# Kernel tuning notes

Hardware: AMD Instinct MI355X
Metric: run time of the kernel (lower is better)

The kernel has to match this reference:

```python
import jax, jax.numpy as jnp
import numpy as np

D_MODEL = 1024
N_HEADS = 16
HEAD_DIM = D_MODEL // N_HEADS
HIDDEN = 4096
EPS = 1e-5


def setup_inputs() -> dict:
    key = jax.random.key(0)
    ks = jax.random.split(key, 16)
    s = 1.0 / np.sqrt(D_MODEL)
    sh = 1.0 / np.sqrt(HIDDEN)
    inp = {
        'x': jax.random.normal(ks[0], (4, 2048, D_MODEL), dtype=jnp.float32),
        'Wq': jax.random.normal(ks[1], (D_MODEL, D_MODEL), dtype=jnp.float32) * s,
        'bq': jnp.zeros((D_MODEL,), jnp.float32),
        'Wk': jax.random.normal(ks[2], (D_MODEL, D_MODEL), dtype=jnp.float32) * s,
        'bk': jnp.zeros((D_MODEL,), jnp.float32),
        'Wv': jax.random.normal(ks[3], (D_MODEL, D_MODEL), dtype=jnp.float32) * s,
        'bv': jnp.zeros((D_MODEL,), jnp.float32),
        'Wo': jax.random.normal(ks[4], (D_MODEL, D_MODEL), dtype=jnp.float32) * s,
        'bo': jnp.zeros((D_MODEL,), jnp.float32),
        'gamma1': jnp.ones((D_MODEL,), jnp.float32),
        'beta1': jnp.zeros((D_MODEL,), jnp.float32),
        'W1': jax.random.normal(ks[5], (D_MODEL, HIDDEN), dtype=jnp.float32) * s,
        'b1': jnp.zeros((HIDDEN,), jnp.float32),
        'W2': jax.random.normal(ks[6], (HIDDEN, D_MODEL), dtype=jnp.float32) * sh,
        'b2': jnp.zeros((D_MODEL,), jnp.float32),
        'gamma2': jnp.ones((D_MODEL,), jnp.float32),
        'beta2': jnp.zeros((D_MODEL,), jnp.float32),
    }
    return inp


def _layernorm(x, gamma, beta):
    mu = jnp.mean(x, axis=-1, keepdims=True)
    var = jnp.mean(jnp.square(x - mu), axis=-1, keepdims=True)
    return (x - mu) * jax.lax.rsqrt(var + EPS) * gamma + beta


def _encoder_layer(x, Wq, bq, Wk, bk, Wv, bv, Wo, bo, gamma1, beta1,
                   W1, b1, W2, b2, gamma2, beta2):
    B, S, _ = x.shape
    # projections -> [B, H, S, Dh]
    def split_heads(t):
        return t.reshape(B, S, N_HEADS, HEAD_DIM).transpose(0, 2, 1, 3)
    q = split_heads(x @ Wq + bq)
    k = split_heads(x @ Wk + bk)
    v = split_heads(x @ Wv + bv)
    scale = 1.0 / jnp.sqrt(jnp.float32(HEAD_DIM))
    scores = jnp.einsum('bhqd,bhkd->bhqk', q, k) * scale
    attn = jax.nn.softmax(scores, axis=-1)
    ctx = jnp.einsum('bhqk,bhkd->bhqd', attn, v)
    ctx = ctx.transpose(0, 2, 1, 3).reshape(B, S, D_MODEL)
    attn_out = ctx @ Wo + bo
    # post-norm residual 1
    h = _layernorm(x + attn_out, gamma1, beta1)
    # MLP with exact (erf) GELU, as torch F.gelu default
    mlp = jax.nn.gelu(h @ W1 + b1, approximate=False) @ W2 + b2
    return _layernorm(h + mlp, gamma2, beta2)


def reference(x, Wq, bq, Wk, bk, Wv, bv, Wo, bo, gamma1, beta1,
              W1, b1, W2, b2, gamma2, beta2):
    return _encoder_layer(x, Wq, bq, Wk, bk, Wv, bv, Wo, bo, gamma1, beta1,
                          W1, b1, W2, b2, gamma2, beta2)
```

## Files before the change

### kernel.cpp

```cpp
#include <hip/hip_runtime.h>
#include <cstdint>
#include <cstddef>

using u16 = unsigned short;
using bf16x8 = __attribute__((ext_vector_type(8))) short;
using f32x4  = __attribute__((ext_vector_type(4))) float;

__device__ __forceinline__ u16 f2bf(float f) {
    union { float f; unsigned u; } v; v.f = f;
    unsigned r = v.u + 0x7fffu + ((v.u >> 16) & 1u);
    return (u16)(r >> 16);
}

__device__ __forceinline__ unsigned cvtpk(float lo, float hi) {
    unsigned r;
    asm("v_cvt_pk_bf16_f32 %0, %1, %2" : "=v"(r) : "v"(lo), "v"(hi));
    return r;
}

__device__ __forceinline__ float fexp2(float x) {
    float r;
    asm("v_exp_f32 %0, %1" : "=v"(r) : "v"(x));
    return r;
}

__device__ __forceinline__ float gelu_f(float x) {
    const float t2 = fminf(x * fmaf(0.10294825f, x * x, 2.3022082f), 80.f);
    const float e  = fexp2(t2);
    return x * e * __frcp_rn(e + 1.0f);
}

__device__ __forceinline__ void gld_lds16(const void* g, void* l) {
    __builtin_amdgcn_global_load_lds(
        (__attribute__((address_space(1))) void*)g,
        (__attribute__((address_space(3))) void*)l, 16, 0, 0);
}

__device__ __forceinline__ f32x4 mfma16(bf16x8 a, bf16x8 b, f32x4 c) {
    return __builtin_amdgcn_mfma_f32_16x16x32_bf16(a, b, c, 0, 0, 0);
}

__global__ __launch_bounds__(256)
void cast_kernel(const float* __restrict__ in, u16* __restrict__ out, int n8) {
    int i = blockIdx.x * 256 + threadIdx.x;
    if (i >= n8) return;
    const float4* p = (const float4*)in;
    float4 a = p[i * 2], b = p[i * 2 + 1];
    ushort4 r0 = make_ushort4(f2bf(a.x), f2bf(a.y), f2bf(a.z), f2bf(a.w));
    ushort4 r1 = make_ushort4(f2bf(b.x), f2bf(b.y), f2bf(b.z), f2bf(b.w));
    ((ushort4*)out)[i * 2]     = r0;
    ((ushort4*)out)[i * 2 + 1] = r1;
}

__global__ __launch_bounds__(256)
void tcast_kernel(const float* __restrict__ in, u16* __restrict__ out, int K, int N,
                  float scale) {
    __shared__ float tile[32][33];
    const int k0 = blockIdx.y * 32, n0 = blockIdx.x * 32;
    const int tx = threadIdx.x & 31, ty = threadIdx.x >> 5;
    #pragma unroll
    for (int r = 0; r < 4; ++r) {
        int k = ty * 4 + r;
        tile[k][tx] = in[(size_t)(k0 + k) * N + n0 + tx];
    }
    __syncthreads();
    #pragma unroll
    for (int r = 0; r < 4; ++r) {
        int n = ty * 4 + r;
        out[(size_t)(n0 + n) * K + k0 + tx] = f2bf(tile[tx][n] * scale);
    }
}

__global__ __launch_bounds__(256)
void bias_concat_kernel(const float* __restrict__ bq, const float* __restrict__ bk,
                        const float* __restrict__ bv, float* __restrict__ out) {
    int i = blockIdx.x * 256 + threadIdx.x;
    if (i >= 3072) return;
    float v;
    if (i < 1024)      v = bq[i] * 0.18033688011112042f;
    else if (i < 2048) v = bk[i - 1024];
    else               v = bv[i - 2048];
    out[i] = v;
}

template <int BM, int EPI>
__global__ __launch_bounds__(512, 1)
void gemm_pipe_kernel(const u16* __restrict__ A, const u16* __restrict__ Bt,
                      const float* __restrict__ bias, void* __restrict__ Cout,
                      int M, int N, int K)
{
    constexpr int AH  = BM * 64;
    constexpr int BH  = 16384;
    constexpr int BUF = 2 * AH + 2 * BH;
    constexpr int LPA = BM / 128;
    constexpr int VMN = LPA + 2;
    constexpr int MR  = BM / 32;
    constexpr int MRH = MR / 2;

    extern __shared__ char smem[];

    const int tid  = threadIdx.x;
    const int wid  = tid >> 6, lane = tid & 63;
    const int l15  = lane & 15, l4 = lane >> 4;
    const int wm   = wid >> 2, wn = wid & 3;

    const int nwg = gridDim.x;
    const int qx = nwg >> 3, rx = nwg & 7;
    const int orig = blockIdx.x;
    const int xcd = orig & 7, jx = orig >> 3;
    const int wgid = (xcd < rx ? xcd * (qx + 1) : rx * (qx + 1) + (xcd - rx) * qx) + jx;
    const int MT = M / BM;
    const int m0 = (wgid % MT) * BM;
    const int n0 = (wgid / MT) * 256;

    const int q0 = tid >> 3, g0 = tid & 7;
    const int u0 = g0 ^ (q0 & 7);
    const int r0 = (q0 << 1) | (u0 >> 2), c80 = u0 & 3;
    const int q1 = q0 + 64;
    const int u1 = g0 ^ (q1 & 7);
    const int r1 = (q1 << 1) | (u1 >> 2), c81 = u1 & 3;
    const u16* aP0 = A  + (size_t)(m0 + r0) * K + c80 * 8;
    const u16* aP1 = A  + (size_t)(m0 + r1) * K + c81 * 8;
    const u16* bP0 = Bt + (size_t)(n0 + r0) * K + c80 * 8;
    const u16* bP1 = Bt + (size_t)(n0 + r1) * K + c81 * 8;
    const int NT = K >> 6;

    auto stageA = [&](int tt, int kk, int nb) {
        char* dst = smem + nb * BUF + kk * AH + tid * 16;
        const int kte = (tt << 6) + (kk << 5);
        gld_lds16(aP0 + kte, dst);
        if constexpr (LPA == 2) gld_lds16(aP1 + kte, dst + 8192);
    };
    auto stageB = [&](int tt, int kk, int nb) {
        char* dst = smem + nb * BUF + 2 * AH + kk * BH + tid * 16;
        const int kte = (tt << 6) + (kk << 5);
        gld_lds16(bP0 + kte, dst);
        gld_lds16(bP1 + kte, dst + 8192);
    };

    auto frag_off = [&](int row) -> int {
        const int q = row >> 1;
        const int u = ((row & 1) << 2) | l4;
        const int g = u ^ (q & 7);
        return q * 128 + g * 16;
    };

    f32x4 acc[MR][4];
    #pragma unroll
    for (int i = 0; i < MR; ++i)
        #pragma unroll
        for (int jj = 0; jj < 4; ++jj) acc[i][jj] = f32x4{0.f, 0.f, 0.f, 0.f};

    stageA(0, 0, 0); stageB(0, 0, 0); stageA(0, 1, 0); stageB(0, 1, 0);
    if constexpr (VMN == 4) asm volatile("s_waitcnt vmcnt(4)" ::: "memory");
    else                    asm volatile("s_waitcnt vmcnt(3)" ::: "memory");
    __builtin_amdgcn_s_barrier();
    asm volatile("" ::: "memory");

    for (int t = 0; t < NT; ++t) {
        const int cur = t & 1, nb = cur ^ 1;
        const int tn = (t + 1 < NT) ? t + 1 : t;
        const char* buf = smem + cur * BUF;
        bf16x8 bfr[4], af[MRH];

        #pragma unroll
        for (int kk = 0; kk < 2; ++kk) {
            #pragma unroll
            for (int fc = 0; fc < 4; ++fc)
                bfr[fc] = *(const bf16x8*)(buf + 2 * AH + kk * BH +
                                           frag_off(wn * 64 + fc * 16 + l15));
            #pragma unroll
            for (int i = 0; i < MRH; ++i)
                af[i] = *(const bf16x8*)(buf + kk * AH +
                                         frag_off(wm * (BM / 2) + i * 16 + l15));
            stageA(tn, kk, nb);
            asm volatile("" ::: "memory");
            __builtin_amdgcn_s_barrier();
            asm volatile("" ::: "memory");
            __builtin_amdgcn_s_setprio(1);
            #pragma unroll
            for (int i = 0; i < MRH; ++i)
                #pragma unroll
                for (int fc = 0; fc < 4; ++fc)
                    acc[i][fc] = mfma16(af[i], bfr[fc], acc[i][fc]);
            __builtin_amdgcn_s_setprio(0);

            #pragma unroll
            for (int i = 0; i < MRH; ++i)
                af[i] = *(const bf16x8*)(buf + kk * AH +
                                         frag_off(wm * (BM / 2) + (MRH + i) * 16 + l15));
            stageB(tn, kk, nb);
            if constexpr (VMN == 4) asm volatile("s_waitcnt vmcnt(4)" ::: "memory");
            else                    asm volatile("s_waitcnt vmcnt(3)" ::: "memory");
            __builtin_amdgcn_s_barrier();
            asm volatile("" ::: "memory");
            __builtin_amdgcn_s_setprio(1);
            #pragma unroll
            for (int i = 0; i < MRH; ++i)
                #pragma unroll
                for (int fc = 0; fc < 4; ++fc)
                    acc[MRH + i][fc] = mfma16(af[i], bfr[fc], acc[MRH + i][fc]);
            __builtin_amdgcn_s_setprio(0);
            asm volatile("" ::: "memory");
        }
    }

    float bv[4];
    #pragma unroll
    for (int fc = 0; fc < 4; ++fc) bv[fc] = bias[n0 + wn * 64 + fc * 16 + l15];
    #pragma unroll
    for (int fr = 0; fr < MR; ++fr) {
        const int rowg = m0 + wm * (BM / 2) + fr * 16 + l4 * 4;
        #pragma unroll
        for (int fc = 0; fc < 4; ++fc) {
            const int colg = n0 + wn * 64 + fc * 16 + l15;
            #pragma unroll
            for (int r = 0; r < 4; ++r) {
                const float v = acc[fr][fc][r] + bv[fc];
                const size_t off = (size_t)(rowg + r) * N + colg;
                if (EPI == 0) ((u16*)Cout)[off] = f2bf(v);
                else          ((u16*)Cout)[off] = f2bf(gelu_f(v));
            }
        }
    }
}

__global__ __launch_bounds__(256)
void vtrans_kernel(const u16* __restrict__ QKV, u16* __restrict__ Vt) {
    __shared__ u16 tile[64][68];
    const int t  = threadIdx.x;
    const int st = blockIdx.x, bh = blockIdx.y;
    const int b  = bh >> 4, h = bh & 15;
    #pragma unroll
    for (int i = 0; i < 2; ++i) {
        int sl = i * 32 + (t >> 3);
        const u16* gp = QKV + ((size_t)b * 2048 + st * 64 + sl) * 3072 + 2048 + h * 64 + (t & 7) * 8;
        ushort4 a = *(const ushort4*)gp;
        ushort4 c = *(const ushort4*)(gp + 4);
        u16* lp = &tile[sl][(t & 7) * 8];
        *(ushort4*)lp       = a;
        *(ushort4*)(lp + 4) = c;
    }
    __syncthreads();
    #pragma unroll
    for (int i = 0; i < 2; ++i) {
        int d  = i * 32 + (t >> 3);
        int s8 = (t & 7) * 8;
        ushort4 o0, o1;
        o0.x = tile[s8 + 0][d]; o0.y = tile[s8 + 1][d]; o0.z = tile[s8 + 2][d]; o0.w = tile[s8 + 3][d];
        o1.x = tile[s8 + 4][d]; o1.y = tile[s8 + 5][d]; o1.z = tile[s8 + 6][d]; o1.w = tile[s8 + 7][d];
        u16* op = Vt + ((size_t)bh * 64 + d) * 2048 + st * 64 + s8;
        *(ushort4*)op       = o0;
        *(ushort4*)(op + 4) = o1;
    }
}

__global__ __launch_bounds__(512)
void attn_kernel(const u16* __restrict__ QKV, const u16* __restrict__ Vt,
                 u16* __restrict__ ctx)
{
    __shared__ u16 smem[24576];

    const int tid = threadIdx.x;
    const int wid = tid >> 6, lane = tid & 63;
    const int l15 = lane & 15, l4 = lane >> 4;
    const int sw  = l15 & 7;
    const int lr  = lane >> 3;
    const int gsrc = ((lane & 7) ^ lr) * 8;
    const int qt = blockIdx.x, bh = blockIdx.y;
    const int b = bh >> 4, h = bh & 15;
    const size_t qrow0 = (size_t)b * 2048 + (size_t)qt * 256;

    u16* const K0 = smem + 16384;
    u16* const V0 = smem + 20480;
    u16* const K1 = smem;
    u16* const V1 = smem + 4096;

    const u16* Qbase = QKV + h * 64;
    const u16* Kbase = QKV + (size_t)b * 2048 * 3072 + 1024 + h * 64;
    const u16* Vbase = Vt + (size_t)bh * 64 * 2048;

    #pragma unroll
    for (int c = 0; c < 4; ++c) {
        const int chunk = wid * 4 + c;
        const int row = chunk * 8 + lr;
        gld_lds16(Qbase + (qrow0 + row) * 3072 + gsrc,
                  (char*)smem + chunk * 1024);
    }

    auto stage_kv = [&](int kt, u16* kb, u16* vb) {
        const int rho = wid * 8 + lr;
        const int krow = (rho & 32) + ((rho & 16) >> 2) + ((rho & 12) << 1) + (rho & 3);
        gld_lds16(Kbase + (size_t)(kt + krow) * 3072 + gsrc,
                  (char*)kb + wid * 1024);
        gld_lds16(Vbase + (size_t)rho * 2048 + kt + gsrc,
                  (char*)vb + wid * 1024);
    };

    stage_kv(0, K0, V0);
    __syncthreads();

    bf16x8 qf[2][2];
    #pragma unroll
    for (int mi = 0; mi < 2; ++mi)
        #pragma unroll
        for (int kk = 0; kk < 2; ++kk)
            qf[mi][kk] = *(const bf16x8*)
                &smem[(size_t)(wid * 32 + mi * 16 + l15) * 64 + (((kk * 4 + l4) ^ sw) * 8)];
    __syncthreads();

    f32x4 accO[2][4] = {};
    f32x4 accL[2] = {};
    const short one_bf = (short)0x3F80;
    const bf16x8 ones = {one_bf, one_bf, one_bf, one_bf,
                         one_bf, one_bf, one_bf, one_bf};

    union U4 { unsigned u[4]; bf16x8 v; };

    auto compute_tile = [&](const u16* kb, const u16* vb) {
        f32x4 st[2][4];
        #pragma unroll
        for (int mi = 0; mi < 2; ++mi)
            #pragma unroll
            for (int ni = 0; ni < 4; ++ni) st[mi][ni] = f32x4{0.f, 0.f, 0.f, 0.f};
        __builtin_amdgcn_s_setprio(1);
        #pragma unroll
        for (int ni = 0; ni < 4; ++ni) {
            bf16x8 kf0 = *(const bf16x8*)&kb[(ni * 16 + l15) * 64 + ((l4 ^ sw) * 8)];
            bf16x8 kf1 = *(const bf16x8*)&kb[(ni * 16 + l15) * 64 + (((4 + l4) ^ sw) * 8)];
            #pragma unroll
            for (int mi = 0; mi < 2; ++mi) {
                st[mi][ni] = mfma16(kf0, qf[mi][0], st[mi][ni]);
                st[mi][ni] = mfma16(kf1, qf[mi][1], st[mi][ni]);
            }
        }
        __builtin_amdgcn_s_setprio(0);

        U4 pb[2][2];
        #pragma unroll
        for (int mi = 0; mi < 2; ++mi) {
            float p[4][4];
            #pragma unroll
            for (int ni = 0; ni < 4; ++ni)
                #pragma unroll
                for (int r = 0; r < 4; ++r)
                    p[ni][r] = fexp2(st[mi][ni][r]);
            #pragma unroll
            for (int ni = 0; ni < 4; ++ni) {
                pb[mi][ni >> 1].u[(ni & 1) * 2 + 0] = cvtpk(p[ni][0], p[ni][1]);
                pb[mi][ni >> 1].u[(ni & 1) * 2 + 1] = cvtpk(p[ni][2], p[ni][3]);
            }
        }

        __builtin_amdgcn_s_setprio(1);
        #pragma unroll
        for (int mi = 0; mi < 2; ++mi) {
            accL[mi] = mfma16(ones, pb[mi][0].v, accL[mi]);
            accL[mi] = mfma16(ones, pb[mi][1].v, accL[mi]);
        }
        #pragma unroll
        for (int di = 0; di < 4; ++di) {
            bf16x8 vf0 = *(const bf16x8*)&vb[(di * 16 + l15) * 64 + ((l4 ^ sw) * 8)];
            bf16x8 vf1 = *(const bf16x8*)&vb[(di * 16 + l15) * 64 + (((4 + l4) ^ sw) * 8)];
            #pragma unroll
            for (int mi = 0; mi < 2; ++mi) {
                accO[mi][di] = mfma16(vf0, pb[mi][0].v, accO[mi][di]);
                accO[mi][di] = mfma16(vf1, pb[mi][1].v, accO[mi][di]);
            }
        }
        __builtin_amdgcn_s_setprio(0);
    };

    for (int it = 0; it < 32; it += 2) {
        if (it + 1 < 32) stage_kv((it + 1) * 64, K1, V1);
        compute_tile(K0, V0);
        __syncthreads();
        if (it + 2 < 32) stage_kv((it + 2) * 64, K0, V0);
        compute_tile(K1, V1);
        __syncthreads();
    }

    #pragma unroll
    for (int mi = 0; mi < 2; ++mi) {
        const float inv = 1.0f / accL[mi][0];
        const size_t q = qrow0 + wid * 32 + mi * 16 + l15;
        #pragma unroll
        for (int di = 0; di < 4; ++di) {
            uint2 w;
            w.x = cvtpk(accO[mi][di][0] * inv, accO[mi][di][1] * inv);
            w.y = cvtpk(accO[mi][di][2] * inv, accO[mi][di][3] * inv);
            *(uint2*)&ctx[q * 1024 + h * 64 + di * 16 + l4 * 4] = w;
        }
    }
}

__global__ __launch_bounds__(256)
void add_ln_kernel(const float* __restrict__ X, const u16* __restrict__ Y,
                   const float* __restrict__ gamma, const float* __restrict__ beta,
                   float* __restrict__ outf, u16* __restrict__ outb)
{
    const int row = blockIdx.x;
    const int t = threadIdx.x;
    const float4 x = ((const float4*)(X + (size_t)row * 1024))[t];
    const ushort4 yb = ((const ushort4*)(Y + (size_t)row * 1024))[t];
    union { unsigned u; float f; } c0, c1, c2, c3;
    c0.u = (unsigned)yb.x << 16; c1.u = (unsigned)yb.y << 16;
    c2.u = (unsigned)yb.z << 16; c3.u = (unsigned)yb.w << 16;
    const float v0 = x.x + c0.f, v1 = x.y + c1.f, v2 = x.z + c2.f, v3 = x.w + c3.f;
    float s  = v0 + v1 + v2 + v3;
    float ss = v0 * v0 + v1 * v1 + v2 * v2 + v3 * v3;
    #pragma unroll
    for (int m = 1; m < 64; m <<= 1) {
        s  += __shfl_xor(s, m, 64);
        ss += __shfl_xor(ss, m, 64);
    }
    __shared__ float red[8];
    const int wid = t >> 6, lane = t & 63;
    if (lane == 0) { red[wid] = s; red[4 + wid] = ss; }
    __syncthreads();
    s  = red[0] + red[1] + red[2] + red[3];
    ss = red[4] + red[5] + red[6] + red[7];
    const float mu  = s * (1.f / 1024.f);
    const float var = ss * (1.f / 1024.f) - mu * mu;
    const float inv = rsqrtf(var + 1e-5f);
    const float4 g  = ((const float4*)gamma)[t];
    const float4 bb = ((const float4*)beta)[t];
    float4 o;
    o.x = (v0 - mu) * inv * g.x + bb.x;
    o.y = (v1 - mu) * inv * g.y + bb.y;
    o.z = (v2 - mu) * inv * g.z + bb.z;
    o.w = (v3 - mu) * inv * g.w + bb.w;
    ((float4*)(outf + (size_t)row * 1024))[t] = o;
    if (outb != nullptr) {
        ushort4 ob = make_ushort4(f2bf(o.x), f2bf(o.y), f2bf(o.z), f2bf(o.w));
        ((ushort4*)(outb + (size_t)row * 1024))[t] = ob;
    }
}

extern "C" void kernel_launch(void* const* d_in, const int* in_sizes, int n_in,
                              void* d_out, int out_size, void* d_ws, size_t ws_size,
                              hipStream_t stream)
{
    (void)in_sizes; (void)n_in; (void)out_size; (void)ws_size;
    const float* x   = (const float*)d_in[0];
    const float* Wq  = (const float*)d_in[1];
    const float* bq  = (const float*)d_in[2];
    const float* Wk  = (const float*)d_in[3];
    const float* bk  = (const float*)d_in[4];
    const float* Wv  = (const float*)d_in[5];
    const float* bv  = (const float*)d_in[6];
    const float* Wo  = (const float*)d_in[7];
    const float* bo  = (const float*)d_in[8];
    const float* g1  = (const float*)d_in[9];
    const float* be1 = (const float*)d_in[10];
    const float* W1  = (const float*)d_in[11];
    const float* b1  = (const float*)d_in[12];
    const float* W2  = (const float*)d_in[13];
    const float* b2  = (const float*)d_in[14];
    const float* g2  = (const float*)d_in[15];
    const float* be2 = (const float*)d_in[16];

    constexpr int M = 8192;
    constexpr int D = 1024;
    constexpr int F = 4096;

    char* ws = (char*)d_ws;
    size_t off = 0;
    auto nxt = [&](size_t bytes) -> char* {
        char* p = ws + off;
        off += (bytes + 255) & ~(size_t)255;
        return p;
    };
    u16*   xb    = (u16*)nxt((size_t)M * D * 2);
    u16*   wqkvt = (u16*)nxt((size_t)3 * D * D * 2);
    u16*   wot   = (u16*)nxt((size_t)D * D * 2);
    u16*   w1t   = (u16*)nxt((size_t)F * D * 2);
    u16*   w2t   = (u16*)nxt((size_t)D * F * 2);
    float* bqkv  = (float*)nxt(3072 * 4);
    u16*   qkv   = (u16*)nxt((size_t)M * 3 * D * 2);
    u16*   Vtb   = (u16*)nxt((size_t)M * D * 2);
    u16*   ctx   = (u16*)nxt((size_t)M * D * 2);
    u16*   attn  = (u16*)nxt((size_t)M * D * 2);
    float* hf    = (float*)nxt((size_t)M * D * 4);
    u16*   hb    = (u16*)nxt((size_t)M * D * 2);
    u16*   t1    = qkv;
    u16*   mlp   = attn;

    constexpr float QS = 0.18033688011112042f;
    cast_kernel<<<dim3(M * D / 8 / 256), dim3(256), 0, stream>>>(x, xb, M * D / 8);
    tcast_kernel<<<dim3(D / 32, D / 32), dim3(256), 0, stream>>>(Wq, wqkvt,             D, D, QS);
    tcast_kernel<<<dim3(D / 32, D / 32), dim3(256), 0, stream>>>(Wk, wqkvt + D * D,     D, D, 1.0f);
    tcast_kernel<<<dim3(D / 32, D / 32), dim3(256), 0, stream>>>(Wv, wqkvt + 2 * D * D, D, D, 1.0f);
    tcast_kernel<<<dim3(D / 32, D / 32), dim3(256), 0, stream>>>(Wo, wot, D, D, 1.0f);
    tcast_kernel<<<dim3(F / 32, D / 32), dim3(256), 0, stream>>>(W1, w1t, D, F, 1.0f);
    tcast_kernel<<<dim3(D / 32, F / 32), dim3(256), 0, stream>>>(W2, w2t, F, D, 1.0f);
    bias_concat_kernel<<<dim3(12), dim3(256), 0, stream>>>(bq, bk, bv, bqkv);

    constexpr size_t LDS128 = 2 * (2 * 128 * 64 + 2 * 16384);
    constexpr size_t LDS256 = 2 * (2 * 256 * 64 + 2 * 16384);

    gemm_pipe_kernel<128, 0><<<dim3((M / 128) * (3 * D / 256)), dim3(512), LDS128, stream>>>(
        xb, wqkvt, bqkv, qkv, M, 3 * D, D);

    vtrans_kernel<<<dim3(2048 / 64, 64), dim3(256), 0, stream>>>(qkv, Vtb);
    attn_kernel<<<dim3(2048 / 256, 64), dim3(512), 0, stream>>>(qkv, Vtb, ctx);

    gemm_pipe_kernel<128, 0><<<dim3((M / 128) * (D / 256)), dim3(512), LDS128, stream>>>(
        ctx, wot, bo, attn, M, D, D);
    add_ln_kernel<<<dim3(M), dim3(256), 0, stream>>>(x, attn, g1, be1, hf, hb);

    gemm_pipe_kernel<256, 2><<<dim3((M / 256) * (F / 256)), dim3(512), LDS256, stream>>>(
        hb, w1t, b1, t1, M, F, D);
    gemm_pipe_kernel<128, 0><<<dim3((M / 128) * (D / 256)), dim3(512), LDS128, stream>>>(
        t1, w2t, b2, mlp, M, D, F);
    add_ln_kernel<<<dim3(M), dim3(256), 0, stream>>>(hf, mlp, g2, be2, (float*)d_out, nullptr);
}
```

Baseline: 399.7 us.

## Triple-buffer GEMM pipeline, unify on 128-row tiles, use bf16 residuals in layernorm

Reworks the GEMM kernel from double to triple LDS buffering, prefetching two k-tiles ahead with a deeper vmcnt wait. This is meant to hide more global-load latency. The GEMM is also fixed at 128-row tiles, so the W1 GEMM now runs at 128 rows instead of 256, which changes grid size and tile reuse. The add+layernorm kernels now read the residual from bf16 buffers (xb and hb) instead of fp32, and the fp32 h buffer is dropped to save memory traffic. This lowers residual precision relative to the reference.

```diff
diff --git a/kernel.cpp b/kernel.cpp
--- a/kernel.cpp
+++ b/kernel.cpp
@@ -10,6 +10,11 @@
     union { float f; unsigned u; } v; v.f = f;
     unsigned r = v.u + 0x7fffu + ((v.u >> 16) & 1u);
     return (u16)(r >> 16);
+}
+
+__device__ __forceinline__ float bf2f(u16 b) {
+    union { unsigned u; float f; } v; v.u = (unsigned)b << 16;
+    return v.f;
 }
 
 __device__ __forceinline__ unsigned cvtpk(float lo, float hi) {
@@ -83,19 +88,16 @@
     out[i] = v;
 }
 
-template <int BM, int EPI>
+template <int EPI>
 __global__ __launch_bounds__(512, 1)
 void gemm_pipe_kernel(const u16* __restrict__ A, const u16* __restrict__ Bt,
                       const float* __restrict__ bias, void* __restrict__ Cout,
                       int M, int N, int K)
 {
-    constexpr int AH  = BM * 64;
+    constexpr int AH  = 8192;
     constexpr int BH  = 16384;
     constexpr int BUF = 2 * AH + 2 * BH;
-    constexpr int LPA = BM / 128;
-    constexpr int VMN = LPA + 2;
-    constexpr int MR  = BM / 32;
-    constexpr int MRH = MR / 2;
+    constexpr int MRH = 2;
 
     extern __shared__ char smem[];
 
@@ -109,8 +111,8 @@
     const int orig = blockIdx.x;
     const int xcd = orig & 7, jx = orig >> 3;
     const int wgid = (xcd < rx ? xcd * (qx + 1) : rx * (qx + 1) + (xcd - rx) * qx) + jx;
-    const int MT = M / BM;
-    const int m0 = (wgid % MT) * BM;
+    const int MT = M / 128;
+    const int m0 = (wgid % MT) * 128;
     const int n0 = (wgid / MT) * 256;
 
     const int q0 = tid >> 3, g0 = tid & 7;
@@ -120,19 +122,16 @@
     const int u1 = g0 ^ (q1 & 7);
     const int r1 = (q1 << 1) | (u1 >> 2), c81 = u1 & 3;
     const u16* aP0 = A  + (size_t)(m0 + r0) * K + c80 * 8;
-    const u16* aP1 = A  + (size_t)(m0 + r1) * K + c81 * 8;
     const u16* bP0 = Bt + (size_t)(n0 + r0) * K + c80 * 8;
     const u16* bP1 = Bt + (size_t)(n0 + r1) * K + c81 * 8;
     const int NT = K >> 6;
 
-    auto stageA = [&](int tt, int kk, int nb) {
-        char* dst = smem + nb * BUF + kk * AH + tid * 16;
-        const int kte = (tt << 6) + (kk << 5);
-        gld_lds16(aP0 + kte, dst);
-        if constexpr (LPA == 2) gld_lds16(aP1 + kte, dst + 8192);
+    auto stageA = [&](int tt, int kk, int bsel) {
+        char* dst = smem + bsel * BUF + kk * AH + tid * 16;
+        gld_lds16(aP0 + (tt << 6) + (kk << 5), dst);
     };
-    auto stageB = [&](int tt, int kk, int nb) {
-        char* dst = smem + nb * BUF + 2 * AH + kk * BH + tid * 16;
+    auto stageB = [&](int tt, int kk, int bsel) {
+        char* dst = smem + bsel * BUF + 2 * AH + kk * BH + tid * 16;
         const int kte = (tt << 6) + (kk << 5);
         gld_lds16(bP0 + kte, dst);
         gld_lds16(bP1 + kte, dst + 8192);
@@ -145,22 +144,23 @@
         return q * 128 + g * 16;
     };
 
-    f32x4 acc[MR][4];
-    #pragma unroll
-    for (int i = 0; i < MR; ++i)
+    f32x4 acc[4][4];
+    #pragma unroll
+    for (int i = 0; i < 4; ++i)
         #pragma unroll
         for (int jj = 0; jj < 4; ++jj) acc[i][jj] = f32x4{0.f, 0.f, 0.f, 0.f};
 
     stageA(0, 0, 0); stageB(0, 0, 0); stageA(0, 1, 0); stageB(0, 1, 0);
-    if constexpr (VMN == 4) asm volatile("s_waitcnt vmcnt(4)" ::: "memory");
-    else                    asm volatile("s_waitcnt vmcnt(3)" ::: "memory");
+    stageA(1, 0, 1); stageB(1, 0, 1); stageA(1, 1, 1); stageB(1, 1, 1);
+    asm volatile("s_waitcnt vmcnt(9)" ::: "memory");
     __builtin_amdgcn_s_barrier();
     asm volatile("" ::: "memory");
 
+    int bsel = 0;
     for (int t = 0; t < NT; ++t) {
-        const int cur = t & 1, nb = cur ^ 1;
-        const int tn = (t + 1 < NT) ? t + 1 : t;
-        const char* buf = smem + cur * BUF;
+        const int tn2 = (t + 2 < NT) ? t + 2 : t;
+        const int nb2 = (bsel + 2) % 3;
+        const char* buf = smem + bsel * BUF;
         bf16x8 bfr[4], af[MRH];
 
         #pragma unroll
@@ -172,8 +172,8 @@
             #pragma unroll
             for (int i = 0; i < MRH; ++i)
                 af[i] = *(const bf16x8*)(buf + kk * AH +
-                                         frag_off(wm * (BM / 2) + i * 16 + l15));
-            stageA(tn, kk, nb);
+                                         frag_off(wm * 64 + i * 16 + l15));
+            stageA(tn2, kk, nb2);
             asm volatile("" ::: "memory");
             __builtin_amdgcn_s_barrier();
             asm volatile("" ::: "memory");
@@ -188,10 +188,9 @@
             #pragma unroll
             for (int i = 0; i < MRH; ++i)
                 af[i] = *(const bf16x8*)(buf + kk * AH +
-                                         frag_off(wm * (BM / 2) + (MRH + i) * 16 + l15));
-            stageB(tn, kk, nb);
-            if constexpr (VMN == 4) asm volatile("s_waitcnt vmcnt(4)" ::: "memory");
-            else                    asm volatile("s_waitcnt vmcnt(3)" ::: "memory");
+                                         frag_off(wm * 64 + (MRH + i) * 16 + l15));
+            stageB(tn2, kk, nb2);
+            asm volatile("s_waitcnt vmcnt(9)" ::: "memory");
             __builtin_amdgcn_s_barrier();
             asm volatile("" ::: "memory");
             __builtin_amdgcn_s_setprio(1);
@@ -203,14 +202,15 @@
             __builtin_amdgcn_s_setprio(0);
             asm volatile("" ::: "memory");
         }
+        bsel = (bsel + 1) % 3;
     }
 
     float bv[4];
     #pragma unroll
     for (int fc = 0; fc < 4; ++fc) bv[fc] = bias[n0 + wn * 64 + fc * 16 + l15];
     #pragma unroll
-    for (int fr = 0; fr < MR; ++fr) {
-        const int rowg = m0 + wm * (BM / 2) + fr * 16 + l4 * 4;
+    for (int fr = 0; fr < 4; ++fr) {
+        const int rowg = m0 + wm * 64 + fr * 16 + l4 * 4;
         #pragma unroll
         for (int fc = 0; fc < 4; ++fc) {
             const int colg = n0 + wn * 64 + fc * 16 + l15;
@@ -395,18 +395,18 @@
 }
 
 __global__ __launch_bounds__(256)
-void add_ln_kernel(const float* __restrict__ X, const u16* __restrict__ Y,
+void add_ln_kernel(const u16* __restrict__ X, const u16* __restrict__ Y,
                    const float* __restrict__ gamma, const float* __restrict__ beta,
                    float* __restrict__ outf, u16* __restrict__ outb)
 {
     const int row = blockIdx.x;
     const int t = threadIdx.x;
-    const float4 x = ((const float4*)(X + (size_t)row * 1024))[t];
+    const ushort4 xb = ((const ushort4*)(X + (size_t)row * 1024))[t];
     const ushort4 yb = ((const ushort4*)(Y + (size_t)row * 1024))[t];
-    union { unsigned u; float f; } c0, c1, c2, c3;
-    c0.u = (unsigned)yb.x << 16; c1.u = (unsigned)yb.y << 16;
-    c2.u = (unsigned)yb.z << 16; c3.u = (unsigned)yb.w << 16;
-    const float v0 = x.x + c0.f, v1 = x.y + c1.f, v2 = x.z + c2.f, v3 = x.w + c3.f;
+    const float v0 = bf2f(xb.x) + bf2f(yb.x);
+    const float v1 = bf2f(xb.y) + bf2f(yb.y);
+    const float v2 = bf2f(xb.z) + bf2f(yb.z);
+    const float v3 = bf2f(xb.w) + bf2f(yb.w);
     float s  = v0 + v1 + v2 + v3;
     float ss = v0 * v0 + v1 * v1 + v2 * v2 + v3 * v3;
     #pragma unroll
@@ -430,7 +430,8 @@
     o.y = (v1 - mu) * inv * g.y + bb.y;
     o.z = (v2 - mu) * inv * g.z + bb.z;
     o.w = (v3 - mu) * inv * g.w + bb.w;
-    ((float4*)(outf + (size_t)row * 1024))[t] = o;
+    if (outf != nullptr)
+        ((float4*)(outf + (size_t)row * 1024))[t] = o;
     if (outb != nullptr) {
         ushort4 ob = make_ushort4(f2bf(o.x), f2bf(o.y), f2bf(o.z), f2bf(o.w));
         ((ushort4*)(outb + (size_t)row * 1024))[t] = ob;
@@ -481,7 +482,6 @@
     u16*   Vtb   = (u16*)nxt((size_t)M * D * 2);
     u16*   ctx   = (u16*)nxt((size_t)M * D * 2);
     u16*   attn  = (u16*)nxt((size_t)M * D * 2);
-    float* hf    = (float*)nxt((size_t)M * D * 4);
     u16*   hb    = (u16*)nxt((size_t)M * D * 2);
     u16*   t1    = qkv;
     u16*   mlp   = attn;
@@ -496,22 +496,21 @@
     tcast_kernel<<<dim3(D / 32, F / 32), dim3(256), 0, stream>>>(W2, w2t, F, D, 1.0f);
     bias_concat_kernel<<<dim3(12), dim3(256), 0, stream>>>(bq, bk, bv, bqkv);
 
-    constexpr size_t LDS128 = 2 * (2 * 128 * 64 + 2 * 16384);
-    constexpr size_t LDS256 = 2 * (2 * 256 * 64 + 2 * 16384);
-
-    gemm_pipe_kernel<128, 0><<<dim3((M / 128) * (3 * D / 256)), dim3(512), LDS128, stream>>>(
+    constexpr size_t LDS3 = 3 * 49152;
+
+    gemm_pipe_kernel<0><<<dim3((M / 128) * (3 * D / 256)), dim3(512), LDS3, stream>>>(
         xb, wqkvt, bqkv, qkv, M, 3 * D, D);
 
     vtrans_kernel<<<dim3(2048 / 64, 64), dim3(256), 0, stream>>>(qkv, Vtb);
     attn_kernel<<<dim3(2048 / 256, 64), dim3(512), 0, stream>>>(qkv, Vtb, ctx);
 
-    gemm_pipe_kernel<128, 0><<<dim3((M / 128) * (D / 256)), dim3(512), LDS128, stream>>>(
+    gemm_pipe_kernel<0><<<dim3((M / 128) * (D / 256)), dim3(512), LDS3, stream>>>(
         ctx, wot, bo, attn, M, D, D);
-    add_ln_kernel<<<dim3(M), dim3(256), 0, stream>>>(x, attn, g1, be1, hf, hb);
-
-    gemm_pipe_kernel<256, 2><<<dim3((M / 256) * (F / 256)), dim3(512), LDS256, stream>>>(
+    add_ln_kernel<<<dim3(M), dim3(256), 0, stream>>>(xb, attn, g1, be1, nullptr, hb);
+
+    gemm_pipe_kernel<2><<<dim3((M / 128) * (F / 256)), dim3(512), LDS3, stream>>>(
         hb, w1t, b1, t1, M, F, D);
-    gemm_pipe_kernel<128, 0><<<dim3((M / 128) * (D / 256)), dim3(512), LDS128, stream>>>(
+    gemm_pipe_kernel<0><<<dim3((M / 128) * (D / 256)), dim3(512), LDS3, stream>>>(
         t1, w2t, b2, mlp, M, D, F);
-    add_ln_kernel<<<dim3(M), dim3(256), 0, stream>>>(hf, mlp, g2, be2, (float*)d_out, nullptr);
-}
+    add_ln_kernel<<<dim3(M), dim3(256), 0, stream>>>(hb, mlp, g2, be2, (float*)d_out, nullptr);
+}
```

New measurement: 402.4 us. No clear change (+0.7%).
